# Performance work log

Hardware: AMD Instinct MI355X
Metric: run time of the kernel (lower is better)

## Reference

```python
import jax, jax.numpy as jnp
import numpy as np

HIDDEN = 1024
RANK = 4
N_TASKS = 5
LORA_SCALING = 1.0 / RANK  # lora_alpha / lora_rank = 1/4
LN_EPS = 1e-5


def setup_inputs() -> dict:
    key = jax.random.key(0)
    ks = jax.random.split(key, 9)
    B, S, D = 16, 2048, HIDDEN
    hidden_states = jax.random.normal(ks[0], (B, S, D), dtype=jnp.float32)
    input_tensor = jax.random.normal(ks[1], (B, S, D), dtype=jnp.float32)
    adapter_mask = jax.random.randint(ks[2], (B,), 0, N_TASKS, dtype=jnp.int32)
    W = jax.random.normal(ks[3], (D, D), dtype=jnp.float32) * 0.02
    b = jax.random.normal(ks[4], (D,), dtype=jnp.float32) * 0.02
    lora_A = jax.random.normal(ks[5], (N_TASKS, RANK, D), dtype=jnp.float32) * 0.02
    lora_B = jax.random.normal(ks[6], (N_TASKS, D, RANK), dtype=jnp.float32) * 0.02
    gamma = jnp.ones((D,), dtype=jnp.float32)
    beta = jnp.zeros((D,), dtype=jnp.float32)
    return {
        "hidden_states": hidden_states,
        "input_tensor": input_tensor,
        "W": W,
        "b": b,
        "lora_A": lora_A,
        "lora_B": lora_B,
        "gamma": gamma,
        "beta": beta,
        "adapter_mask": adapter_mask,
    }


def _layernorm(x, gamma, beta):
    mu = jnp.mean(x, axis=-1, keepdims=True)
    xc = x - mu
    var = jnp.mean(xc * xc, axis=-1, keepdims=True)
    return xc * jax.lax.rsqrt(var + LN_EPS) * gamma + beta


def reference(hidden_states, input_tensor, W, b, lora_A, lora_B, gamma, beta, adapter_mask):
    # Base dense projection (first self.dense call)
    h1 = jnp.einsum("bsd,ed->bse", hidden_states, W) + b  # [B,S,D]
    # Per-task LoRA-parametrized dense applied to the projected states
    # (the source loops over unique tasks with gather/scatter; vectorized here
    #  by gathering each batch row's adapter).
    base2 = jnp.einsum("bsd,ed->bse", h1, W) + b  # [B,S,D]
    A_b = lora_A[adapter_mask]  # [B, r, D]
    B_b = lora_B[adapter_mask]  # [B, D, r]
    low = jnp.einsum("bsd,brd->bsr", h1, A_b)  # [B,S,r]
    delta = jnp.einsum("bsr,bdr->bsd", low, B_b)  # [B,S,D]
    h2 = base2 + LORA_SCALING * delta
    # dropout is identity in eval / p=0; residual + LayerNorm
    return _layernorm(h2 + input_tensor, gamma, beta)
```

## Files before the change

kernel.cpp:

```cpp
#include <hip/hip_runtime.h>
#include <hip/hip_bf16.h>
#include <stdint.h>

#define D_HID 1024
#define M_TOT 32768
#define LN_EPS 1e-5f

typedef __bf16 bf16x8 __attribute__((ext_vector_type(8)));
typedef float f32x4 __attribute__((ext_vector_type(4)));
typedef unsigned short u16;
typedef u16 u16x8 __attribute__((ext_vector_type(8)));
typedef u16 u16x4v __attribute__((ext_vector_type(4)));

__device__ __forceinline__ float bf2f(u16 x) {
  union { unsigned int u; float f; } c; c.u = ((unsigned int)x) << 16; return c.f;
}
__device__ __forceinline__ u16 f2bf(float f) {
  union { __bf16 h; u16 u; } c; c.h = (__bf16)f; return c.u;
}
__device__ __forceinline__ u16x8 cvt8(const float* g) {
  float4 f0 = *(const float4*)g;
  float4 f1 = *(const float4*)(g + 4);
  u16x8 v;
  v[0] = f2bf(f0.x); v[1] = f2bf(f0.y); v[2] = f2bf(f0.z); v[3] = f2bf(f0.w);
  v[4] = f2bf(f1.x); v[5] = f2bf(f1.y); v[6] = f2bf(f1.z); v[7] = f2bf(f1.w);
  return v;
}
__device__ __forceinline__ void gld16(const u16* g, u16* lds_wave_base) {
  __builtin_amdgcn_global_load_lds(
      (__attribute__((address_space(1))) unsigned int*)g,
      (__attribute__((address_space(3))) unsigned int*)lds_wave_base, 16, 0, 0);
}

__global__ __launch_bounds__(256) void s1_prep(
    const float* __restrict__ hs, u16* __restrict__ hs_bf,
    const float* __restrict__ W, u16* __restrict__ hi, u16* __restrict__ lo,
    u16* __restrict__ hiT, u16* __restrict__ loT,
    const float* __restrict__ lA, u16* __restrict__ lAh, u16* __restrict__ lAl) {
  __shared__ float tile[32][33];
  const int bid = blockIdx.x, tid = threadIdx.x;
  if (bid < 2048) {
    int i = bid * 256 + tid;
#pragma unroll
    for (int it = 0; it < 8; ++it, i += 2048 * 256)
      *(u16x8*)(hs_bf + (size_t)i * 8) = cvt8(hs + (size_t)i * 8);
    return;
  }
  if (bid >= 3072) {
    const int b = bid - 3072;
    for (int i = tid; i < 16 * 1024; i += 256) {
      const int r = b * 16 + (i >> 10), c = i & 1023;
      const float v = (r < 20) ? lA[(size_t)r * 1024 + c] : 0.f;
      const u16 h = f2bf(v);
      lAh[(size_t)r * 1024 + c] = h;
      lAl[(size_t)r * 1024 + c] = f2bf(v - bf2f(h));
    }
    return;
  }
  const int rb = bid - 2048;
  const int bj = rb & 31, bi = rb >> 5;
  const int tx = tid & 31, ty = tid >> 5;
#pragma unroll
  for (int r0 = 0; r0 < 32; r0 += 8) {
    const int r = r0 + ty;
    const size_t o = (size_t)(bi * 32 + r) * D_HID + bj * 32 + tx;
    const float v = W[o];
    tile[r][tx] = v;
    const u16 h = f2bf(v);
    hi[o] = h; lo[o] = f2bf(v - bf2f(h));
  }
  __syncthreads();
#pragma unroll
  for (int r0 = 0; r0 < 32; r0 += 8) {
    const int r = r0 + ty;
    const float v = tile[tx][r];
    const size_t o = (size_t)(bj * 32 + r) * D_HID + bi * 32 + tx;
    const u16 h = f2bf(v);
    hiT[o] = h; loT[o] = f2bf(v - bf2f(h));
  }
}

__global__ __launch_bounds__(256, 1) void s2_gemm(
    const u16* __restrict__ Ah, const u16* __restrict__ Al,
    const u16* __restrict__ Bh, const u16* __restrict__ Bl,
    const u16* __restrict__ lAh, const u16* __restrict__ lAl,
    float* __restrict__ C, float* __restrict__ A2) {
  __shared__ __align__(16) u16 sAh[128 * 32], sAl[128 * 32];
  __shared__ __align__(16) u16 sBh[128 * 32], sBl[128 * 32];
  const int bid = blockIdx.x, tid = threadIdx.x, wave = tid >> 6, lane = tid & 63;
  const int by = bid >> 3, bx = bid & 7;
  const bool isA2 = (by == 8);
  const u16* Asrc_h = isA2 ? lAh : Ah;
  const u16* Asrc_l = isA2 ? lAl : Al;
  const int rowbase = isA2 ? 0 : by * 128;
  const int srow = tid >> 2, scol = (tid & 3) * 8;
  size_t aOff = (size_t)(rowbase + srow) * D_HID + scol;
  size_t bOff = (size_t)(bx * 128 + srow) * D_HID + scol;
  const int wb = wave * 512;
  const int wm = wave >> 1, wn = wave & 1;
  const int mrow = lane & 15, quad = lane >> 4;
  const int fA = (wm * 64 + mrow) * 32 + quad * 8;
  const int fB = (wn * 64 + mrow) * 32 + quad * 8;
  f32x4 acc[4][4];
#pragma unroll
  for (int i = 0; i < 4; ++i)
#pragma unroll
    for (int jn = 0; jn < 4; ++jn) acc[i][jn] = (f32x4){0.f, 0.f, 0.f, 0.f};
  for (int k0 = 0; k0 < D_HID; k0 += 32) {
    __syncthreads();
    gld16(Asrc_h + aOff, sAh + wb); gld16(Asrc_h + aOff + 64 * D_HID, sAh + wb + 2048);
    gld16(Asrc_l + aOff, sAl + wb); gld16(Asrc_l + aOff + 64 * D_HID, sAl + wb + 2048);
    gld16(Bh + bOff, sBh + wb); gld16(Bh + bOff + 64 * D_HID, sBh + wb + 2048);
    gld16(Bl + bOff, sBl + wb); gld16(Bl + bOff + 64 * D_HID, sBl + wb + 2048);
    aOff += 32; bOff += 32;
    __syncthreads();
    bf16x8 ah[4], al4[4], bh[4], bl4[4];
#pragma unroll
    for (int m = 0; m < 4; ++m) {
      ah[m]  = *(const bf16x8*)(sAh + fA + m * 512);
      al4[m] = *(const bf16x8*)(sAl + fA + m * 512);
    }
#pragma unroll
    for (int n = 0; n < 4; ++n) {
      bh[n]  = *(const bf16x8*)(sBh + fB + n * 512);
      bl4[n] = *(const bf16x8*)(sBl + fB + n * 512);
    }
#pragma unroll
    for (int m = 0; m < 4; ++m)
#pragma unroll
      for (int n = 0; n < 4; ++n) {
        acc[m][n] = __builtin_amdgcn_mfma_f32_16x16x32_bf16(ah[m],  bh[n],  acc[m][n], 0, 0, 0);
        acc[m][n] = __builtin_amdgcn_mfma_f32_16x16x32_bf16(al4[m], bh[n],  acc[m][n], 0, 0, 0);
        acc[m][n] = __builtin_amdgcn_mfma_f32_16x16x32_bf16(ah[m],  bl4[n], acc[m][n], 0, 0, 0);
      }
  }
  const int nBase = bx * 128 + wn * 64;
#pragma unroll
  for (int m = 0; m < 4; ++m)
#pragma unroll
    for (int n = 0; n < 4; ++n) {
      const int nn = nBase + n * 16 + mrow;
#pragma unroll
      for (int r = 0; r < 4; ++r) {
        const int lr = wm * 64 + m * 16 + quad * 4 + r;
        if (!isA2) {
          C[(size_t)(by * 128 + lr) * D_HID + nn] = acc[m][n][r];
        } else if (lr < 20) {
          A2[(size_t)lr * D_HID + nn] = acc[m][n][r];
        }
      }
    }
}

__global__ __launch_bounds__(256) void weff_beff(
    const float* __restrict__ Wc, const float* __restrict__ A2,
    const float* __restrict__ lB, const float* __restrict__ lA,
    const float* __restrict__ W, const float* __restrict__ bvec,
    u16* __restrict__ Weff, float* __restrict__ beff) {
  const int n = blockIdx.x, t = blockIdx.y, tid = threadIdx.x;
  const int wave = tid >> 6, lane = tid & 63;
  float br[4];
#pragma unroll
  for (int r = 0; r < 4; ++r) br[r] = lB[(size_t)t * 4096 + n * 4 + r];
  float4 v = *(const float4*)(Wc + (size_t)n * D_HID + tid * 4);
#pragma unroll
  for (int r = 0; r < 4; ++r) {
    const float4 a2 = *(const float4*)(A2 + (size_t)(t * 4 + r) * D_HID + tid * 4);
    const float s = 0.25f * br[r];
    v.x += s * a2.x; v.y += s * a2.y; v.z += s * a2.z; v.w += s * a2.w;
  }
  u16x4v o; o[0] = f2bf(v.x); o[1] = f2bf(v.y); o[2] = f2bf(v.z); o[3] = f2bf(v.w);
  *(u16x4v*)(Weff + (size_t)t * 1048576 + (size_t)n * D_HID + tid * 4) = o;
  const float4 bb = *(const float4*)(bvec + tid * 4);
  float p[5];
  {
    const float4 wr = *(const float4*)(W + (size_t)n * D_HID + tid * 4);
    p[0] = wr.x * bb.x + wr.y * bb.y + wr.z * bb.z + wr.w * bb.w;
  }
#pragma unroll
  for (int r = 0; r < 4; ++r) {
    const float4 ar = *(const float4*)(lA + (size_t)(t * 4 + r) * D_HID + tid * 4);
    p[1 + r] = ar.x * bb.x + ar.y * bb.y + ar.z * bb.z + ar.w * bb.w;
  }
#pragma unroll
  for (int m = 1; m < 64; m <<= 1)
#pragma unroll
    for (int jj = 0; jj < 5; ++jj) p[jj] += __shfl_xor(p[jj], m);
  __shared__ float red[4][5];
  if (lane == 0)
#pragma unroll
    for (int jj = 0; jj < 5; ++jj) red[wave][jj] = p[jj];
  __syncthreads();
  if (tid == 0) {
    float P = 0.f, Cr[4] = {0.f, 0.f, 0.f, 0.f};
#pragma unroll
    for (int w = 0; w < 4; ++w) {
      P += red[w][0];
#pragma unroll
      for (int r = 0; r < 4; ++r) Cr[r] += red[w][1 + r];
    }
    const float e = br[0]*Cr[0] + br[1]*Cr[1] + br[2]*Cr[2] + br[3]*Cr[3];
    beff[t * D_HID + n] = P + bvec[n] + 0.25f * e;
  }
}

__global__ __launch_bounds__(512, 1) void gemm_main(
    const u16* __restrict__ Ag, const u16* __restrict__ Wf,
    const float* __restrict__ beff, const float* __restrict__ resid,
    const int* __restrict__ mask, float* __restrict__ out) {
  __shared__ __align__(16) u16 sAf[2 * 16384];
  __shared__ __align__(16) u16 sBf[2 * 16384];
  const int tid = threadIdx.x, wave = tid >> 6, lane = tid & 63;
  const int L = blockIdx.x;
  const int xcd = L & 7, j = L >> 3;
  const int bx = j & 3;
  const int by = xcd * 16 + (j >> 2);
  const int task = mask[by >> 3];
  const u16* Bg = Wf + (size_t)task * (D_HID * D_HID);

  const int acol = ((lane & 7) ^ (lane >> 3)) * 8;
  const int aBase = (by * 256 + wave * 8 + (lane >> 3)) * D_HID + acol;
  const int bBase = (bx * 256 + wave * 8 + (lane >> 3)) * D_HID + acol;

  auto stageA = [&](int ktar, int half) {
#pragma unroll
    for (int q = 0; q < 2; ++q)
      gld16(Ag + (aBase + ktar * 64 + half * 131072 + q * 65536),
            sAf + ((ktar & 1) * 16384 + half * 8192 + q * 4096 + wave * 512));
  };
  auto stageB = [&](int ktar, int half) {
#pragma unroll
    for (int q = 0; q < 2; ++q)
      gld16(Bg + (bBase + ktar * 64 + half * 131072 + q * 65536),
            sBf + ((ktar & 1) * 16384 + half * 8192 + q * 4096 + wave * 512));
  };

  const int wm = wave >> 2, wn = wave & 3;
  const int l15 = lane & 15, quad = lane >> 4, l7 = lane & 7;
  const int vA0 = (wm * 128 + l15) * 64 + ((quad ^ l7) * 8);
  const int vB0 = (wn * 64 + l15) * 64 + ((quad ^ l7) * 8);

  f32x4 acc[8][4];
#pragma unroll
  for (int i = 0; i < 8; ++i)
#pragma unroll
    for (int jn = 0; jn < 4; ++jn) acc[i][jn] = (f32x4){0.f, 0.f, 0.f, 0.f};

  stageB(0, 0); stageB(0, 1); stageA(0, 0); stageA(0, 1);
  stageB(1, 0); stageA(1, 0);
  asm volatile("s_waitcnt vmcnt(4)" ::: "memory");
  __builtin_amdgcn_s_barrier();
  __builtin_amdgcn_sched_barrier(0);

  bf16x8 a[4][2], b[4][2];
#pragma unroll 1
  for (int k2 = 0; k2 < 8; ++k2) {
#pragma unroll
    for (int par = 0; par < 2; ++par) {
      const int kt = k2 * 2 + par;
      const u16* pA = sAf + par * 16384;
      const u16* pB = sBf + par * 16384;
      const bool st01 = (par == 0) || (k2 < 7);
      const bool st23 = (k2 < 7);

#pragma unroll
      for (int m4 = 0; m4 < 4; ++m4) {
        a[m4][0] = *(const bf16x8*)(pA + (vA0 + m4 * 1024));
        a[m4][1] = *(const bf16x8*)(pA + ((vA0 ^ 32) + m4 * 1024));
      }
#pragma unroll
      for (int n2 = 0; n2 < 2; ++n2) {
        b[n2][0] = *(const bf16x8*)(pB + (vB0 + n2 * 1024));
        b[n2][1] = *(const bf16x8*)(pB + ((vB0 ^ 32) + n2 * 1024));
      }
      if (st01) stageB(kt + 1, 1);
      __builtin_amdgcn_s_barrier();
      asm volatile("s_waitcnt lgkmcnt(0)" ::: "memory");
      __builtin_amdgcn_sched_barrier(0);
      __builtin_amdgcn_s_setprio(1);
#pragma unroll
      for (int m4 = 0; m4 < 4; ++m4)
#pragma unroll
        for (int n2 = 0; n2 < 2; ++n2)
#pragma unroll
          for (int kk = 0; kk < 2; ++kk)
            acc[m4][n2] = __builtin_amdgcn_mfma_f32_16x16x32_bf16(
                a[m4][kk], b[n2][kk], acc[m4][n2], 0, 0, 0);
      __builtin_amdgcn_s_setprio(0);
      __builtin_amdgcn_s_barrier();
      __builtin_amdgcn_sched_barrier(0);

#pragma unroll
      for (int n2 = 0; n2 < 2; ++n2) {
        b[2 + n2][0] = *(const bf16x8*)(pB + (vB0 + (2 + n2) * 1024));
        b[2 + n2][1] = *(const bf16x8*)(pB + ((vB0 ^ 32) + (2 + n2) * 1024));
      }
      if (st01) stageA(kt + 1, 1);
      __builtin_amdgcn_s_barrier();
      asm volatile("s_waitcnt lgkmcnt(0)" ::: "memory");
      __builtin_amdgcn_sched_barrier(0);
      __builtin_amdgcn_s_setprio(1);
#pragma unroll
      for (int m4 = 0; m4 < 4; ++m4)
#pragma unroll
        for (int n2 = 0; n2 < 2; ++n2)
#pragma unroll
          for (int kk = 0; kk < 2; ++kk)
            acc[m4][2 + n2] = __builtin_amdgcn_mfma_f32_16x16x32_bf16(
                a[m4][kk], b[2 + n2][kk], acc[m4][2 + n2], 0, 0, 0);
      __builtin_amdgcn_s_setprio(0);
      __builtin_amdgcn_s_barrier();
      __builtin_amdgcn_sched_barrier(0);

#pragma unroll
      for (int m4 = 0; m4 < 4; ++m4) {
        a[m4][0] = *(const bf16x8*)(pA + (vA0 + (4 + m4) * 1024));
        a[m4][1] = *(const bf16x8*)(pA + ((vA0 ^ 32) + (4 + m4) * 1024));
      }
      if (st23) stageB(kt + 2, 0);
      __builtin_amdgcn_s_barrier();
      asm volatile("s_waitcnt lgkmcnt(0)" ::: "memory");
      __builtin_amdgcn_sched_barrier(0);
      __builtin_amdgcn_s_setprio(1);
#pragma unroll
      for (int m4 = 0; m4 < 4; ++m4)
#pragma unroll
        for (int n2 = 0; n2 < 2; ++n2)
#pragma unroll
          for (int kk = 0; kk < 2; ++kk)
            acc[4 + m4][n2] = __builtin_amdgcn_mfma_f32_16x16x32_bf16(
                a[m4][kk], b[n2][kk], acc[4 + m4][n2], 0, 0, 0);
      __builtin_amdgcn_s_setprio(0);
      __builtin_amdgcn_s_barrier();
      __builtin_amdgcn_sched_barrier(0);

      if (st23) stageA(kt + 2, 0);
      if (par == 0) {
        if (k2 < 7) { asm volatile("s_waitcnt vmcnt(4)" ::: "memory"); }
        else        { asm volatile("s_waitcnt vmcnt(0)" ::: "memory"); }
      } else {
        if (k2 < 7) { asm volatile("s_waitcnt vmcnt(4)" ::: "memory"); }
      }
      __builtin_amdgcn_s_barrier();
      asm volatile("s_waitcnt lgkmcnt(0)" ::: "memory");
      __builtin_amdgcn_sched_barrier(0);
      __builtin_amdgcn_s_setprio(1);
#pragma unroll
      for (int m4 = 0; m4 < 4; ++m4)
#pragma unroll
        for (int n2 = 0; n2 < 2; ++n2)
#pragma unroll
          for (int kk = 0; kk < 2; ++kk)
            acc[4 + m4][2 + n2] = __builtin_amdgcn_mfma_f32_16x16x32_bf16(
                a[m4][kk], b[2 + n2][kk], acc[4 + m4][2 + n2], 0, 0, 0);
      __builtin_amdgcn_s_setprio(0);
      __builtin_amdgcn_s_barrier();
      __builtin_amdgcn_sched_barrier(0);
    }
  }

  const float* bb = beff + task * D_HID;
  const size_t mBase = (size_t)by * 256 + wm * 128;
  const int nb0 = bx * 256 + wn * 64;
#pragma unroll
  for (int mf = 0; mf < 8; ++mf)
#pragma unroll
    for (int nf = 0; nf < 4; ++nf) {
      const int n = nb0 + nf * 16 + l15;
      const float bval = bb[n];
#pragma unroll
      for (int r = 0; r < 4; ++r) {
        const size_t m = mBase + mf * 16 + quad * 4 + r;
        out[m * D_HID + n] = acc[mf][nf][r] + bval + resid[m * D_HID + n];
      }
    }
}

__global__ __launch_bounds__(256) void ln4(float* __restrict__ io,
                                           const float* __restrict__ gamma,
                                           const float* __restrict__ beta) {
  const int row = blockIdx.x * 4 + (threadIdx.x >> 6);
  const int lane = threadIdx.x & 63;
  float* p = io + (size_t)row * D_HID + lane * 16;
  float4 v0 = ((const float4*)p)[0], v1 = ((const float4*)p)[1];
  float4 v2 = ((const float4*)p)[2], v3 = ((const float4*)p)[3];
  float s = v0.x + v0.y + v0.z + v0.w + v1.x + v1.y + v1.z + v1.w
          + v2.x + v2.y + v2.z + v2.w + v3.x + v3.y + v3.z + v3.w;
  float q = v0.x*v0.x + v0.y*v0.y + v0.z*v0.z + v0.w*v0.w
          + v1.x*v1.x + v1.y*v1.y + v1.z*v1.z + v1.w*v1.w
          + v2.x*v2.x + v2.y*v2.y + v2.z*v2.z + v2.w*v2.w
          + v3.x*v3.x + v3.y*v3.y + v3.z*v3.z + v3.w*v3.w;
#pragma unroll
  for (int m = 1; m < 64; m <<= 1) { s += __shfl_xor(s, m); q += __shfl_xor(q, m); }
  const float mu  = s * (1.f / (float)D_HID);
  const float var = q * (1.f / (float)D_HID) - mu * mu;
  const float inv = rsqrtf(var + LN_EPS);
  const float4* gp = (const float4*)(gamma + lane * 16);
  const float4* bp = (const float4*)(beta + lane * 16);
  float4 g, bbv, o;
#define LNW(k, vk) \
  g = gp[k]; bbv = bp[k]; \
  o.x = (vk.x - mu) * inv * g.x + bbv.x; o.y = (vk.y - mu) * inv * g.y + bbv.y; \
  o.z = (vk.z - mu) * inv * g.z + bbv.z; o.w = (vk.w - mu) * inv * g.w + bbv.w; \
  ((float4*)p)[k] = o;
  LNW(0, v0) LNW(1, v1) LNW(2, v2) LNW(3, v3)
#undef LNW
}

extern "C" void kernel_launch(void* const* d_in, const int* in_sizes, int n_in,
                              void* d_out, int out_size, void* d_ws, size_t ws_size,
                              hipStream_t stream) {
  const float* hs    = (const float*)d_in[0];
  const float* inp   = (const float*)d_in[1];
  const float* W     = (const float*)d_in[2];
  const float* b     = (const float*)d_in[3];
  const float* lA    = (const float*)d_in[4];
  const float* lB    = (const float*)d_in[5];
  const float* gamma = (const float*)d_in[6];
  const float* beta  = (const float*)d_in[7];
  const int*   mask  = (const int*)d_in[8];
  float* out = (float*)d_out;

  char* wsb = (char*)d_ws;
  u16*   hs_bf = (u16*)wsb;
  float* Wc    = (float*)(wsb + 67108864);
  u16*   weff  = (u16*)(wsb + 71303168);
  u16*   Whi   = weff;
  u16*   Wlo   = weff + 1048576;
  u16*   WhiT  = weff + 2097152;
  u16*   WloT  = weff + 3145728;
  u16*   lAh   = weff + 4194304;
  u16*   lAl   = weff + 4325376;
  float* A2    = (float*)(wsb + 81788928);
  float* beff  = (float*)(wsb + 81871360);

  s1_prep<<<3080, 256, 0, stream>>>(hs, hs_bf, W, Whi, Wlo, WhiT, WloT, lA, lAh, lAl);
  s2_gemm<<<72, 256, 0, stream>>>(Whi, Wlo, WhiT, WloT, lAh, lAl, Wc, A2);
  weff_beff<<<dim3(1024, 5), 256, 0, stream>>>(Wc, A2, lB, lA, W, b, weff, beff);
  gemm_main<<<512, 512, 0, stream>>>(hs_bf, weff, beff, inp, mask, out);
  ln4<<<M_TOT / 4, 256, 0, stream>>>(out, gamma, beta);
}
```

Measured before the change: 548.3 us.

## Shrink W·W precompute tiles to 64x64 and move residual add into LayerNorm

```diff
diff --git a/kernel.cpp b/kernel.cpp
--- a/kernel.cpp
+++ b/kernel.cpp
@@ -80,71 +80,73 @@
   }
 }
 
-__global__ __launch_bounds__(256, 1) void s2_gemm(
+__global__ __launch_bounds__(256) void s2_gemm(
     const u16* __restrict__ Ah, const u16* __restrict__ Al,
     const u16* __restrict__ Bh, const u16* __restrict__ Bl,
     const u16* __restrict__ lAh, const u16* __restrict__ lAl,
     float* __restrict__ C, float* __restrict__ A2) {
-  __shared__ __align__(16) u16 sAh[128 * 32], sAl[128 * 32];
-  __shared__ __align__(16) u16 sBh[128 * 32], sBl[128 * 32];
-  const int bid = blockIdx.x, tid = threadIdx.x, wave = tid >> 6, lane = tid & 63;
-  const int by = bid >> 3, bx = bid & 7;
-  const bool isA2 = (by == 8);
-  const u16* Asrc_h = isA2 ? lAh : Ah;
-  const u16* Asrc_l = isA2 ? lAl : Al;
-  const int rowbase = isA2 ? 0 : by * 128;
-  const int srow = tid >> 2, scol = (tid & 3) * 8;
-  size_t aOff = (size_t)(rowbase + srow) * D_HID + scol;
-  size_t bOff = (size_t)(bx * 128 + srow) * D_HID + scol;
-  const int wb = wave * 512;
+  __shared__ __align__(16) u16 smem[4][64 * 32];
+  const int bid = blockIdx.x, tid = threadIdx.x;
+  const int wave = tid >> 6, lane = tid & 63;
+  const int by = bid >> 4, bx = bid & 15;
+  const bool isA2 = (by == 16);
+  const u16* Asel_h = isA2 ? lAh : Ah;
+  const u16* Asel_l = isA2 ? lAl : Al;
+  const int arow0 = isA2 ? 0 : by * 64;
+  const u16* gsel = (wave == 0) ? Asel_h : (wave == 1) ? Asel_l
+                  : (wave == 2) ? Bh : Bl;
+  const int rb = (wave < 2) ? arow0 : bx * 64;
+  const u16* gp = gsel + (size_t)(rb + (lane >> 2)) * D_HID + (lane & 3) * 8;
+  u16* sb = &smem[wave][0];
+
+  const int l15 = lane & 15, quad = lane >> 4;
   const int wm = wave >> 1, wn = wave & 1;
-  const int mrow = lane & 15, quad = lane >> 4;
-  const int fA = (wm * 64 + mrow) * 32 + quad * 8;
-  const int fB = (wn * 64 + mrow) * 32 + quad * 8;
-  f32x4 acc[4][4];
-#pragma unroll
-  for (int i = 0; i < 4; ++i)
-#pragma unroll
-    for (int jn = 0; jn < 4; ++jn) acc[i][jn] = (f32x4){0.f, 0.f, 0.f, 0.f};
+  const int fA = (wm * 32 + l15) * 32 + quad * 8;
+  const int fB = (wn * 32 + l15) * 32 + quad * 8;
+  f32x4 acc[2][2];
+#pragma unroll
+  for (int m = 0; m < 2; ++m)
+#pragma unroll
+    for (int n = 0; n < 2; ++n) acc[m][n] = (f32x4){0.f, 0.f, 0.f, 0.f};
+
   for (int k0 = 0; k0 < D_HID; k0 += 32) {
     __syncthreads();
-    gld16(Asrc_h + aOff, sAh + wb); gld16(Asrc_h + aOff + 64 * D_HID, sAh + wb + 2048);
-    gld16(Asrc_l + aOff, sAl + wb); gld16(Asrc_l + aOff + 64 * D_HID, sAl + wb + 2048);
-    gld16(Bh + bOff, sBh + wb); gld16(Bh + bOff + 64 * D_HID, sBh + wb + 2048);
-    gld16(Bl + bOff, sBl + wb); gld16(Bl + bOff + 64 * D_HID, sBl + wb + 2048);
-    aOff += 32; bOff += 32;
+#pragma unroll
+    for (int q = 0; q < 4; ++q)
+      gld16(gp + (size_t)q * 16 * D_HID, sb + q * 512);
+    gp += 32;
     __syncthreads();
-    bf16x8 ah[4], al4[4], bh[4], bl4[4];
-#pragma unroll
-    for (int m = 0; m < 4; ++m) {
-      ah[m]  = *(const bf16x8*)(sAh + fA + m * 512);
-      al4[m] = *(const bf16x8*)(sAl + fA + m * 512);
-    }
-#pragma unroll
-    for (int n = 0; n < 4; ++n) {
-      bh[n]  = *(const bf16x8*)(sBh + fB + n * 512);
-      bl4[n] = *(const bf16x8*)(sBl + fB + n * 512);
-    }
-#pragma unroll
-    for (int m = 0; m < 4; ++m)
-#pragma unroll
-      for (int n = 0; n < 4; ++n) {
-        acc[m][n] = __builtin_amdgcn_mfma_f32_16x16x32_bf16(ah[m],  bh[n],  acc[m][n], 0, 0, 0);
-        acc[m][n] = __builtin_amdgcn_mfma_f32_16x16x32_bf16(al4[m], bh[n],  acc[m][n], 0, 0, 0);
-        acc[m][n] = __builtin_amdgcn_mfma_f32_16x16x32_bf16(ah[m],  bl4[n], acc[m][n], 0, 0, 0);
-      }
-  }
-  const int nBase = bx * 128 + wn * 64;
-#pragma unroll
-  for (int m = 0; m < 4; ++m)
-#pragma unroll
-    for (int n = 0; n < 4; ++n) {
-      const int nn = nBase + n * 16 + mrow;
+    bf16x8 ahf[2], alf[2], bhf[2], blf[2];
+#pragma unroll
+    for (int m = 0; m < 2; ++m) {
+      ahf[m] = *(const bf16x8*)(&smem[0][fA + m * 512]);
+      alf[m] = *(const bf16x8*)(&smem[1][fA + m * 512]);
+    }
+#pragma unroll
+    for (int n = 0; n < 2; ++n) {
+      bhf[n] = *(const bf16x8*)(&smem[2][fB + n * 512]);
+      blf[n] = *(const bf16x8*)(&smem[3][fB + n * 512]);
+    }
+#pragma unroll
+    for (int m = 0; m < 2; ++m)
+#pragma unroll
+      for (int n = 0; n < 2; ++n) {
+        acc[m][n] = __builtin_amdgcn_mfma_f32_16x16x32_bf16(ahf[m], bhf[n], acc[m][n], 0, 0, 0);
+        acc[m][n] = __builtin_amdgcn_mfma_f32_16x16x32_bf16(alf[m], bhf[n], acc[m][n], 0, 0, 0);
+        acc[m][n] = __builtin_amdgcn_mfma_f32_16x16x32_bf16(ahf[m], blf[n], acc[m][n], 0, 0, 0);
+      }
+  }
+  const int nn0 = bx * 64 + wn * 32;
+#pragma unroll
+  for (int m = 0; m < 2; ++m)
+#pragma unroll
+    for (int n = 0; n < 2; ++n) {
+      const int nn = nn0 + n * 16 + l15;
 #pragma unroll
       for (int r = 0; r < 4; ++r) {
-        const int lr = wm * 64 + m * 16 + quad * 4 + r;
+        const int lr = wm * 32 + m * 16 + quad * 4 + r;
         if (!isA2) {
-          C[(size_t)(by * 128 + lr) * D_HID + nn] = acc[m][n][r];
+          C[(size_t)(by * 64 + lr) * D_HID + nn] = acc[m][n][r];
         } else if (lr < 20) {
           A2[(size_t)lr * D_HID + nn] = acc[m][n][r];
         }
@@ -206,8 +208,8 @@
 
 __global__ __launch_bounds__(512, 1) void gemm_main(
     const u16* __restrict__ Ag, const u16* __restrict__ Wf,
-    const float* __restrict__ beff, const float* __restrict__ resid,
-    const int* __restrict__ mask, float* __restrict__ out) {
+    const float* __restrict__ beff, const int* __restrict__ mask,
+    float* __restrict__ out) {
   __shared__ __align__(16) u16 sAf[2 * 16384];
   __shared__ __align__(16) u16 sBf[2 * 16384];
   const int tid = threadIdx.x, wave = tid >> 6, lane = tid & 63;
@@ -371,19 +373,27 @@
 #pragma unroll
       for (int r = 0; r < 4; ++r) {
         const size_t m = mBase + mf * 16 + quad * 4 + r;
-        out[m * D_HID + n] = acc[mf][nf][r] + bval + resid[m * D_HID + n];
+        out[m * D_HID + n] = acc[mf][nf][r] + bval;
       }
     }
 }
 
 __global__ __launch_bounds__(256) void ln4(float* __restrict__ io,
+                                           const float* __restrict__ resid,
                                            const float* __restrict__ gamma,
                                            const float* __restrict__ beta) {
   const int row = blockIdx.x * 4 + (threadIdx.x >> 6);
   const int lane = threadIdx.x & 63;
   float* p = io + (size_t)row * D_HID + lane * 16;
+  const float* rp = resid + (size_t)row * D_HID + lane * 16;
   float4 v0 = ((const float4*)p)[0], v1 = ((const float4*)p)[1];
   float4 v2 = ((const float4*)p)[2], v3 = ((const float4*)p)[3];
+  float4 r0 = ((const float4*)rp)[0], r1 = ((const float4*)rp)[1];
+  float4 r2 = ((const float4*)rp)[2], r3 = ((const float4*)rp)[3];
+  v0.x += r0.x; v0.y += r0.y; v0.z += r0.z; v0.w += r0.w;
+  v1.x += r1.x; v1.y += r1.y; v1.z += r1.z; v1.w += r1.w;
+  v2.x += r2.x; v2.y += r2.y; v2.z += r2.z; v2.w += r2.w;
+  v3.x += r3.x; v3.y += r3.y; v3.z += r3.z; v3.w += r3.w;
   float s = v0.x + v0.y + v0.z + v0.w + v1.x + v1.y + v1.z + v1.w
           + v2.x + v2.y + v2.z + v2.w + v3.x + v3.y + v3.z + v3.w;
   float q = v0.x*v0.x + v0.y*v0.y + v0.z*v0.z + v0.w*v0.w
@@ -435,8 +445,8 @@
   float* beff  = (float*)(wsb + 81871360);
 
   s1_prep<<<3080, 256, 0, stream>>>(hs, hs_bf, W, Whi, Wlo, WhiT, WloT, lA, lAh, lAl);
-  s2_gemm<<<72, 256, 0, stream>>>(Whi, Wlo, WhiT, WloT, lAh, lAl, Wc, A2);
+  s2_gemm<<<272, 256, 0, stream>>>(Whi, Wlo, WhiT, WloT, lAh, lAl, Wc, A2);
   weff_beff<<<dim3(1024, 5), 256, 0, stream>>>(Wc, A2, lB, lA, W, b, weff, beff);
-  gemm_main<<<512, 512, 0, stream>>>(hs_bf, weff, beff, inp, mask, out);
-  ln4<<<M_TOT / 4, 256, 0, stream>>>(out, gamma, beta);
-}
+  gemm_main<<<512, 512, 0, stream>>>(hs_bf, weff, beff, mask, out);
+  ln4<<<M_TOT / 4, 256, 0, stream>>>(out, inp, gamma, beta);
+}
```

Result: faster. 504.7 us (-8.0%).
